# Kernel tuning notes

Hardware: AMD Instinct MI355X
Metric: run time of the kernel (lower is better)

## Reference

```python
import jax, jax.numpy as jnp
import numpy as np

N = 8192
IN = 128   # in_channels
CH = 64    # conv_ch


def setup_inputs() -> dict:
    key = jax.random.key(0)
    ks = jax.random.split(key, 8)
    p = lambda k, shape: jax.random.normal(k, shape, jnp.float32) * 0.02
    return {
        "x": jax.random.normal(ks[0], (N, IN), jnp.float32),
        "edge_index": jax.random.randint(ks[1], (N, N), 0, 2, jnp.int32),
        "W1": p(ks[2], (IN, CH)),      "b1": jnp.zeros((CH,), jnp.float32),
        "W2": p(ks[3], (CH, 2 * CH)),  "b2": jnp.zeros((2 * CH,), jnp.float32),
        "We": p(ks[4], (2 * CH, CH)),  "be": jnp.zeros((CH,), jnp.float32),
        "Wd1": p(ks[5], (2 * CH, CH)), "bd1": jnp.zeros((CH,), jnp.float32),
        "Wd2": p(ks[6], (CH, IN)),     "bd2": jnp.zeros((IN,), jnp.float32),
    }


def _norm_adj(edge_index):
    # PyG GCNConv: A_hat = A + I (self loops appended), sym norm D^-1/2 A_hat D^-1/2
    A = (edge_index != 0).astype(jnp.float32)
    A = A + jnp.eye(A.shape[0], dtype=jnp.float32)
    deg = A.sum(axis=1)
    dinv = jnp.where(deg > 0.0, jax.lax.rsqrt(deg), 0.0)
    return dinv[:, None] * A * dinv[None, :]  # [N, N]


def _gcn(nadj, x, W, b):
    return nadj @ (x @ W) + b


def _lrelu(v):
    return jax.nn.leaky_relu(v, 0.01)  # torch default negative_slope


def reference(x, edge_index, W1, b1, W2, b2, We, be, Wd1, bd1, Wd2, bd2):
    nadj = _norm_adj(edge_index)
    h = _lrelu(_gcn(nadj, x, W1, b1))          # [N, CH]
    z = _lrelu(_gcn(nadj, h, W2, b2))          # [N, 2*CH]
    re = _lrelu(_gcn(nadj, z, We, be))         # [N, CH]
    recon_edge = jax.nn.sigmoid(re @ re.T)     # [N, N]
    xd = _lrelu(_gcn(nadj, z, Wd1, bd1))       # [N, CH]
    x_out = _lrelu(_gcn(nadj, xd, Wd2, bd2))   # [N, IN]
    return (recon_edge, x_out, z)
```

## Files before the change

### kernel.cpp

```cpp
#include <hip/hip_runtime.h>
#include <hip/hip_bf16.h>
#include <stdint.h>

typedef unsigned short u16;
typedef unsigned char u8;
typedef unsigned int u32;
typedef __attribute__((ext_vector_type(8))) short frag8;
typedef __attribute__((ext_vector_type(4))) float f4;

#define N8K 8192
#define SK 8
#define NKT 256


__device__ __forceinline__ u16 f2bf(float f) {
  union { float f; unsigned u; } v; v.f = f;
  return (u16)((v.u + 0x7FFFu + ((v.u >> 16) & 1u)) >> 16);
}
__device__ __forceinline__ float lrelu(float v) { return v > 0.f ? v : 0.01f * v; }

__device__ __forceinline__ void expand4(u32 w, u32& o0, u32& o1) {
  u32 hi = __builtin_amdgcn_perm(0u, 0x00403F00u, w);
  u32 lo = __builtin_amdgcn_perm(0u, 0x00008000u, w);
  o0 = __builtin_amdgcn_perm(hi, lo, 0x05010400u);
  o1 = __builtin_amdgcn_perm(hi, lo, 0x07030602u);
}

__global__ __launch_bounds__(256) void k_deg(const int* __restrict__ e,
                                             u8* __restrict__ at,
                                             float* __restrict__ dinv) {
  int Rt = blockIdx.x;
  int t = threadIdx.x;
  int rl = t & 15;
  int row = Rt * 16 + rl;
  int tg = t >> 4;
  int diagT = row >> 5;
  int cnt = 0;
  __shared__ int cs[256];
  for (int p = 0; p < 16; ++p) {
    int T = tg + 16 * p;
    const int4* src = (const int4*)(e + (size_t)row * N8K + T * 32);
    u32 w[8];
#pragma unroll
    for (int q8 = 0; q8 < 8; ++q8) {
      int4 v = src[q8];
      u32 c0 = (v.x != 0), c1 = (v.y != 0), c2 = (v.z != 0), c3 = (v.w != 0);
      cnt += (int)(c0 + c1 + c2 + c3);
      w[q8] = c0 | (c1 << 8) | (c2 << 16) | (c3 << 24);
    }
    if (T == diagT) {
      int d = row & 31;
      w[d >> 2] += 1u << (8 * (d & 3));
      cnt += 1;
    }
    u8* dst = at + ((size_t)(Rt * NKT + T) * 64 + rl) * 8;
#pragma unroll
    for (int q = 0; q < 4; ++q) {
      uint2 u; u.x = w[2 * q]; u.y = w[2 * q + 1];
      *(uint2*)(dst + (size_t)(16 * q) * 8) = u;
    }
  }
  cs[t] = cnt;
  __syncthreads();
  if (t < 16) {
    int s = 0;
#pragma unroll
    for (int g = 0; g < 16; ++g) s += cs[t + 16 * g];
    dinv[Rt * 16 + t] = 1.0f / sqrtf((float)s);
  }
}

__global__ __launch_bounds__(256, 2) void k_sgemm(const u16* __restrict__ Xt,
                                                  const float* __restrict__ Xf,
                                                  int KT,
                                                  const float* __restrict__ Wa, int wacols,
                                                  const float* __restrict__ Wb,
                                                  const float* __restrict__ dinv,
                                                  u16* __restrict__ Pt) {
  __shared__ __attribute__((aligned(16))) u16 Wt[8 * 4 * 64 * 8];
  int t = threadIdx.x, mt = blockIdx.x;
  int lane = t & 63, wave = t >> 6;
  int units = 8 * KT * 64;
  for (int u = t; u < units; u += 256) {
    int l = u & 63, T = (u >> 6) % KT, nt = (u >> 6) / KT;
    int n = nt * 16 + (l & 15);
    int k0 = T * 32 + (l >> 4) * 8;
    u16 tmp[8];
#pragma unroll
    for (int j = 0; j < 8; ++j) {
      int k = k0 + j;
      float v = (n < wacols) ? Wa[k * wacols + n] : (Wb ? Wb[k * 64 + (n - 64)] : 0.f);
      tmp[j] = f2bf(v);
    }
    *(uint4*)&Wt[(size_t)u * 8] = *(const uint4*)tmp;
  }
  __syncthreads();
  int wm = (wave >> 1) * 64, wn = (wave & 1) * 64;
  int fm = lane & 15, q = lane >> 4;
  f4 acc[4][4];
#pragma unroll
  for (int m = 0; m < 4; ++m)
#pragma unroll
    for (int n = 0; n < 4; ++n) acc[m][n] = (f4){0.f, 0.f, 0.f, 0.f};
  for (int T = 0; T < KT; ++T) {
    frag8 a[4], b[4];
#pragma unroll
    for (int m = 0; m < 4; ++m) {
      int Rt = mt * 8 + (wm >> 4) + m;
      if (Xf) {
        const float* px = Xf + (size_t)(Rt * 16 + fm) * (KT * 32) + T * 32 + q * 8;
        float4 v0 = *(const float4*)px, v1 = *(const float4*)(px + 4);
        u16 tmp[8] = {f2bf(v0.x), f2bf(v0.y), f2bf(v0.z), f2bf(v0.w),
                      f2bf(v1.x), f2bf(v1.y), f2bf(v1.z), f2bf(v1.w)};
        a[m] = *(const frag8*)tmp;
      } else {
        a[m] = *(const frag8*)(Xt + ((size_t)(Rt * KT + T) * 64 + lane) * 8);
      }
    }
#pragma unroll
    for (int n = 0; n < 4; ++n)
      b[n] = *(const frag8*)&Wt[((size_t)(((wn >> 4) + n) * KT + T) * 64 + lane) * 8];
#pragma unroll
    for (int m = 0; m < 4; ++m)
#pragma unroll
      for (int n = 0; n < 4; ++n)
        acc[m][n] = __builtin_amdgcn_mfma_f32_16x16x32_bf16(a[m], b[n], acc[m][n], 0, 0, 0);
  }
#pragma unroll
  for (int m = 0; m < 4; ++m) {
    int ibase = mt * 128 + wm + 16 * m + q * 4;
    float d0 = dinv[ibase], d1 = dinv[ibase + 1], d2 = dinv[ibase + 2], d3 = dinv[ibase + 3];
#pragma unroll
    for (int n = 0; n < 4; ++n) {
      u32 lo = (u32)f2bf(d0 * acc[m][n][0]) | ((u32)f2bf(d1 * acc[m][n][1]) << 16);
      u32 hi = (u32)f2bf(d2 * acc[m][n][2]) | ((u32)f2bf(d3 * acc[m][n][3]) << 16);
      u32 plo = __shfl_xor(lo, 16, 64);
      u32 phi = __shfl_xor(hi, 16, 64);
      if ((q & 1) == 0) {
        uint4 u; u.x = lo; u.y = hi; u.z = plo; u.w = phi;
        int gi = mt * 128 + wm + 16 * m + (q >> 1) * 8;
        int T2 = gi >> 5;
        int lB = fm + 16 * ((gi >> 3) & 3);
        int nt = (wn >> 4) + n;
        *(uint4*)(Pt + ((size_t)(nt * NKT + T2) * 64 + lB) * 8) = u;
      }
    }
  }
}

__global__ __launch_bounds__(256, 3) void k_bgemm(const u8* __restrict__ At,
                                                  const u16* __restrict__ Bt,
                                                  float* __restrict__ Ctmp) {
  int t = threadIdx.x;
  int mt = blockIdx.x, ks = blockIdx.y;
  int lane = t & 63, wave = t >> 6;
  int wm = (wave >> 1) * 64, wn = (wave & 1) * 64;
  f4 acc[4][4];
#pragma unroll
  for (int m = 0; m < 4; ++m)
#pragma unroll
    for (int n = 0; n < 4; ++n) acc[m][n] = (f4){0.f, 0.f, 0.f, 0.f};

  const int T0 = ks * 32;
  const u8*  Ab = At + ((size_t)((mt * 8 + (wm >> 4)) * NKT + T0) * 64 + lane) * 8;
  const u16* Bb = Bt + ((size_t)(((wn >> 4)) * NKT + T0) * 64 + lane) * 8;

#pragma unroll 2
  for (int T = 0; T < 32; ++T) {
    frag8 a[4], b[4];
#pragma unroll
    for (int m = 0; m < 4; ++m) {
      uint2 w = *(const uint2*)(Ab + (size_t)m * (NKT * 512) + (size_t)T * 512);
      uint4 r;
      expand4(w.x, r.x, r.y);
      expand4(w.y, r.z, r.w);
      a[m] = *(const frag8*)&r;
    }
#pragma unroll
    for (int n = 0; n < 4; ++n)
      b[n] = *(const frag8*)(Bb + (size_t)n * (NKT * 512) + (size_t)T * 512);
#pragma unroll
    for (int m = 0; m < 4; ++m)
#pragma unroll
      for (int n = 0; n < 4; ++n)
        acc[m][n] = __builtin_amdgcn_mfma_f32_16x16x32_bf16(a[m], b[n], acc[m][n], 0, 0, 0);
  }

  float* Co = Ctmp + (size_t)ks * (N8K * 128);
  int fm = lane & 15, rbase = (lane >> 4) * 4;
#pragma unroll
  for (int m = 0; m < 4; ++m) {
    int i0 = mt * 128 + wm + 16 * m + rbase;
#pragma unroll
    for (int n = 0; n < 4; ++n) {
      int c = wn + 16 * n + fm;
#pragma unroll
      for (int r = 0; r < 4; ++r) Co[(size_t)(i0 + r) * 128 + c] = acc[m][n][r];
    }
  }
}

__global__ __launch_bounds__(256) void k_epi(const float* __restrict__ Ctmp,
                                             const float* __restrict__ dinv,
                                             const float* __restrict__ bA,
                                             const float* __restrict__ bB,
                                             float* __restrict__ outF,
                                             u16* __restrict__ o1,
                                             u16* __restrict__ o2, int mode) {
  int idx = blockIdx.x * 256 + threadIdx.x;
  int i = idx >> 4, c8 = idx & 15;
  if (mode == 1 && c8 >= 8) return;
  int c0 = c8 * 8;
  float v[8];
#pragma unroll
  for (int j = 0; j < 8; ++j) v[j] = 0.f;
#pragma unroll
  for (int k = 0; k < SK; ++k) {
    const float4* p = (const float4*)(Ctmp + (size_t)k * (N8K * 128) + (size_t)i * 128 + c0);
    float4 x0 = p[0], x1 = p[1];
    v[0] += x0.x; v[1] += x0.y; v[2] += x0.z; v[3] += x0.w;
    v[4] += x1.x; v[5] += x1.y; v[6] += x1.z; v[7] += x1.w;
  }
  float di = dinv[i];
  u16 ob[8];
  if (mode == 3 && c8 >= 8) {
    int cl = c0 - 64;
#pragma unroll
    for (int j = 0; j < 8; ++j) ob[j] = f2bf(lrelu(di * v[j] + bB[cl + j]));
    int T = (c8 - 8) >> 2, l = (i & 15) + 16 * ((c8 - 8) & 3);
    *(uint4*)(o2 + ((size_t)((i >> 4) * 2 + T) * 64 + l) * 8) = *(const uint4*)ob;
    return;
  }
#pragma unroll
  for (int j = 0; j < 8; ++j) v[j] = lrelu(di * v[j] + bA[c0 + j]);
  if (mode == 4) {
    float4* po = (float4*)(outF + (size_t)i * 128 + c0);
    po[0] = (float4){v[0], v[1], v[2], v[3]};
    po[1] = (float4){v[4], v[5], v[6], v[7]};
    return;
  }
#pragma unroll
  for (int j = 0; j < 8; ++j) ob[j] = f2bf(v[j]);
  int KTo = (mode == 2) ? 4 : 2;
  int T = c8 >> 2, l = (i & 15) + 16 * (c8 & 3);
  *(uint4*)(o1 + ((size_t)((i >> 4) * KTo + T) * 64 + l) * 8) = *(const uint4*)ob;
  if (mode == 2) {
    float4* po = (float4*)(outF + (size_t)i * 128 + c0);
    po[0] = (float4){v[0], v[1], v[2], v[3]};
    po[1] = (float4){v[4], v[5], v[6], v[7]};
  }
}

__global__ __launch_bounds__(256, 4) void k_recon(const u16* __restrict__ ret,
                                                  float* __restrict__ out) {
  int t = threadIdx.x;
  int bi = blockIdx.x, bj = blockIdx.y;
  int lane = t & 63, wave = t >> 6;
  int wm = (wave >> 1) * 64, wn = (wave & 1) * 64;
  int fm = lane & 15;
  f4 acc[4][4];
#pragma unroll
  for (int m = 0; m < 4; ++m)
#pragma unroll
    for (int n = 0; n < 4; ++n) acc[m][n] = (f4){0.f, 0.f, 0.f, 0.f};
#pragma unroll
  for (int T = 0; T < 2; ++T) {
    frag8 a[4], b[4];
#pragma unroll
    for (int m = 0; m < 4; ++m)
      a[m] = *(const frag8*)(ret + ((size_t)((bi * 8 + (wm >> 4) + m) * 2 + T) * 64 + lane) * 8);
#pragma unroll
    for (int n = 0; n < 4; ++n)
      b[n] = *(const frag8*)(ret + ((size_t)((bj * 8 + (wn >> 4) + n) * 2 + T) * 64 + lane) * 8);
#pragma unroll
    for (int m = 0; m < 4; ++m)
#pragma unroll
      for (int n = 0; n < 4; ++n)
        acc[m][n] = __builtin_amdgcn_mfma_f32_16x16x32_bf16(a[m], b[n], acc[m][n], 0, 0, 0);
  }
  int rbase = (lane >> 4) * 4;
#pragma unroll
  for (int m = 0; m < 4; ++m) {
#pragma unroll
    for (int n = 0; n < 4; ++n) {
      int gj = bj * 128 + wn + 16 * n + fm;
#pragma unroll
      for (int r = 0; r < 4; ++r) {
        int gi = bi * 128 + wm + 16 * m + rbase + r;
        float ex = __builtin_amdgcn_exp2f(acc[m][n][r] * -1.442695041f);
        out[(size_t)gi * N8K + gj] = __builtin_amdgcn_rcpf(1.0f + ex);
      }
    }
  }
}

extern "C" void kernel_launch(void* const* d_in, const int* in_sizes, int n_in,
                              void* d_out, int out_size, void* d_ws, size_t ws_size,
                              hipStream_t stream) {
  const float* x   = (const float*)d_in[0];
  const int*   e   = (const int*)d_in[1];
  const float* W1  = (const float*)d_in[2];
  const float* b1  = (const float*)d_in[3];
  const float* W2  = (const float*)d_in[4];
  const float* b2  = (const float*)d_in[5];
  const float* We  = (const float*)d_in[6];
  const float* be  = (const float*)d_in[7];
  const float* Wd1 = (const float*)d_in[8];
  const float* bd1 = (const float*)d_in[9];
  const float* Wd2 = (const float*)d_in[10];
  const float* bd2 = (const float*)d_in[11];

  float* out       = (float*)d_out;
  float* out_recon = out;
  float* out_x     = out + 67108864;
  float* out_z     = out + 67108864 + 1048576;

  u8*    at   = (u8*)d_out;
  float* Ctmp = out + 16777216;

  char* ws = (char*)d_ws;
  float* dinv = (float*)(ws);
  u16* Pt  = (u16*)(ws + 32768);
  u16* ht  = (u16*)(ws + 32768 + 2097152);
  u16* zt  = (u16*)(ws + 32768 + 3145728);
  u16* ret = (u16*)(ws + 32768 + 5242880);
  u16* xdt = (u16*)(ws + 32768 + 6291456);

  k_deg<<<512, 256, 0, stream>>>(e, at, dinv);

  k_sgemm<<<64, 256, 0, stream>>>(nullptr, x, 4, W1, 64, nullptr, dinv, Pt);
  k_bgemm<<<dim3(64, SK), 256, 0, stream>>>(at, Pt, Ctmp);
  k_epi<<<512, 256, 0, stream>>>(Ctmp, dinv, b1, nullptr, nullptr, ht, nullptr, 1);

  k_sgemm<<<64, 256, 0, stream>>>(ht, nullptr, 2, W2, 128, nullptr, dinv, Pt);
  k_bgemm<<<dim3(64, SK), 256, 0, stream>>>(at, Pt, Ctmp);
  k_epi<<<512, 256, 0, stream>>>(Ctmp, dinv, b2, nullptr, out_z, zt, nullptr, 2);

  k_sgemm<<<64, 256, 0, stream>>>(zt, nullptr, 4, We, 64, Wd1, dinv, Pt);
  k_bgemm<<<dim3(64, SK), 256, 0, stream>>>(at, Pt, Ctmp);
  k_epi<<<512, 256, 0, stream>>>(Ctmp, dinv, be, bd1, nullptr, ret, xdt, 3);

  k_sgemm<<<64, 256, 0, stream>>>(xdt, nullptr, 2, Wd2, 128, nullptr, dinv, Pt);
  k_bgemm<<<dim3(64, SK), 256, 0, stream>>>(at, Pt, Ctmp);
  k_epi<<<512, 256, 0, stream>>>(Ctmp, dinv, bd2, nullptr, out_x, nullptr, nullptr, 4);

  k_recon<<<dim3(64, 64), 256, 0, stream>>>(ret, out_recon);
}
```

Before: 686.1 us.

## Fuse split-K epilogue with next layer's feature-weight GEMM

Replaces the separate epilogue kernels (split-K reduction, bias, leaky ReLU, bf16 pack) and the following small GEMM with one fused kernel. The activated tile is staged in shared memory and fed directly to MFMA, which removes three launches and the global round-trips for the intermediate h, z and xd buffers. In exchange, the reduction now runs on only 64 blocks instead of 512, which may underuse memory bandwidth on a large GPU.

```diff
diff --git a/kernel.cpp b/kernel.cpp
--- a/kernel.cpp
+++ b/kernel.cpp
@@ -70,18 +70,15 @@
   }
 }
 
-__global__ __launch_bounds__(256, 2) void k_sgemm(const u16* __restrict__ Xt,
-                                                  const float* __restrict__ Xf,
-                                                  int KT,
-                                                  const float* __restrict__ Wa, int wacols,
-                                                  const float* __restrict__ Wb,
-                                                  const float* __restrict__ dinv,
-                                                  u16* __restrict__ Pt) {
+__global__ __launch_bounds__(256, 2) void k_sgemm1(const float* __restrict__ Xf,
+                                                   const float* __restrict__ Wa,
+                                                   const float* __restrict__ dinv,
+                                                   u16* __restrict__ Pt) {
+  const int KT = 4;
   __shared__ __attribute__((aligned(16))) u16 Wt[8 * 4 * 64 * 8];
   int t = threadIdx.x, mt = blockIdx.x;
   int lane = t & 63, wave = t >> 6;
-  int units = 8 * KT * 64;
-  for (int u = t; u < units; u += 256) {
+  for (int u = t; u < 8 * KT * 64; u += 256) {
     int l = u & 63, T = (u >> 6) % KT, nt = (u >> 6) / KT;
     int n = nt * 16 + (l & 15);
     int k0 = T * 32 + (l >> 4) * 8;
@@ -89,7 +86,7 @@
 #pragma unroll
     for (int j = 0; j < 8; ++j) {
       int k = k0 + j;
-      float v = (n < wacols) ? Wa[k * wacols + n] : (Wb ? Wb[k * 64 + (n - 64)] : 0.f);
+      float v = (n < 64) ? Wa[k * 64 + n] : 0.f;
       tmp[j] = f2bf(v);
     }
     *(uint4*)&Wt[(size_t)u * 8] = *(const uint4*)tmp;
@@ -107,15 +104,11 @@
 #pragma unroll
     for (int m = 0; m < 4; ++m) {
       int Rt = mt * 8 + (wm >> 4) + m;
-      if (Xf) {
-        const float* px = Xf + (size_t)(Rt * 16 + fm) * (KT * 32) + T * 32 + q * 8;
-        float4 v0 = *(const float4*)px, v1 = *(const float4*)(px + 4);
-        u16 tmp[8] = {f2bf(v0.x), f2bf(v0.y), f2bf(v0.z), f2bf(v0.w),
-                      f2bf(v1.x), f2bf(v1.y), f2bf(v1.z), f2bf(v1.w)};
-        a[m] = *(const frag8*)tmp;
-      } else {
-        a[m] = *(const frag8*)(Xt + ((size_t)(Rt * KT + T) * 64 + lane) * 8);
-      }
+      const float* px = Xf + (size_t)(Rt * 16 + fm) * 128 + T * 32 + q * 8;
+      float4 v0 = *(const float4*)px, v1 = *(const float4*)(px + 4);
+      u16 tmp[8] = {f2bf(v0.x), f2bf(v0.y), f2bf(v0.z), f2bf(v0.w),
+                    f2bf(v1.x), f2bf(v1.y), f2bf(v1.z), f2bf(v1.w)};
+      a[m] = *(const frag8*)tmp;
     }
 #pragma unroll
     for (int n = 0; n < 4; ++n)
@@ -200,16 +193,132 @@
   }
 }
 
-__global__ __launch_bounds__(256) void k_epi(const float* __restrict__ Ctmp,
-                                             const float* __restrict__ dinv,
-                                             const float* __restrict__ bA,
-                                             const float* __restrict__ bB,
-                                             float* __restrict__ outF,
-                                             u16* __restrict__ o1,
-                                             u16* __restrict__ o2, int mode) {
+__global__ __launch_bounds__(256, 2) void k_fuse(const float* __restrict__ Ctmp,
+                                                 const float* __restrict__ dinv,
+                                                 const float* __restrict__ bE,
+                                                 const float* __restrict__ bE2,
+                                                 float* __restrict__ outZ,
+                                                 u16* __restrict__ retG,
+                                                 int mode,
+                                                 const float* __restrict__ Wa, int wacols,
+                                                 const float* __restrict__ Wb,
+                                                 u16* __restrict__ Pt) {
+  __shared__ __attribute__((aligned(16))) u16 Xs[8 * 4 * 64 * 8];
+  __shared__ __attribute__((aligned(16))) u16 Wt[8 * 4 * 64 * 8];
+  int t = threadIdx.x, mt = blockIdx.x;
+  int lane = t & 63, wave = t >> 6;
+  const int KT = (mode == 2) ? 4 : 2;
+
+  int C8 = (mode == 1) ? 8 : 16;
+  int totalU = 128 * C8;
+  for (int u0 = t; u0 < totalU; u0 += 256) {
+    int i = (mode == 1) ? (u0 >> 3) : (u0 >> 4);
+    int c8 = (mode == 1) ? (u0 & 7) : (u0 & 15);
+    int gi = mt * 128 + i;
+    int c0 = c8 * 8;
+    float v[8];
+#pragma unroll
+    for (int j = 0; j < 8; ++j) v[j] = 0.f;
+#pragma unroll
+    for (int k = 0; k < SK; ++k) {
+      const float4* p = (const float4*)(Ctmp + (size_t)k * (N8K * 128) + (size_t)gi * 128 + c0);
+      float4 x0 = p[0], x1 = p[1];
+      v[0] += x0.x; v[1] += x0.y; v[2] += x0.z; v[3] += x0.w;
+      v[4] += x1.x; v[5] += x1.y; v[6] += x1.z; v[7] += x1.w;
+    }
+    float di = dinv[gi];
+    u16 ob[8];
+    if (mode == 3 && c8 < 8) {
+#pragma unroll
+      for (int j = 0; j < 8; ++j) ob[j] = f2bf(lrelu(di * v[j] + bE[c0 + j]));
+      int T = c8 >> 2, l = (i & 15) + 16 * (c8 & 3);
+      *(uint4*)(retG + ((size_t)((gi >> 4) * 2 + T) * 64 + l) * 8) = *(const uint4*)ob;
+    } else if (mode == 3) {
+      int cl = c0 - 64;
+#pragma unroll
+      for (int j = 0; j < 8; ++j) ob[j] = f2bf(lrelu(di * v[j] + bE2[cl + j]));
+      int cp = c8 - 8;
+      int T = cp >> 2, l = (i & 15) + 16 * (cp & 3);
+      *(uint4*)&Xs[(((i >> 4) * 2 + T) * 64 + l) * 8] = *(const uint4*)ob;
+    } else {
+#pragma unroll
+      for (int j = 0; j < 8; ++j) v[j] = lrelu(di * v[j] + bE[c0 + j]);
+#pragma unroll
+      for (int j = 0; j < 8; ++j) ob[j] = f2bf(v[j]);
+      int T = c8 >> 2, l = (i & 15) + 16 * (c8 & 3);
+      *(uint4*)&Xs[(((i >> 4) * KT + T) * 64 + l) * 8] = *(const uint4*)ob;
+      if (mode == 2) {
+        float4* po = (float4*)(outZ + (size_t)gi * 128 + c0);
+        po[0] = (float4){v[0], v[1], v[2], v[3]};
+        po[1] = (float4){v[4], v[5], v[6], v[7]};
+      }
+    }
+  }
+
+  for (int u = t; u < 8 * KT * 64; u += 256) {
+    int l = u & 63, T = (u >> 6) % KT, nt = (u >> 6) / KT;
+    int n = nt * 16 + (l & 15);
+    int k0 = T * 32 + (l >> 4) * 8;
+    u16 tmp[8];
+#pragma unroll
+    for (int j = 0; j < 8; ++j) {
+      int k = k0 + j;
+      float v = (n < wacols) ? Wa[k * wacols + n] : (Wb ? Wb[k * 64 + (n - 64)] : 0.f);
+      tmp[j] = f2bf(v);
+    }
+    *(uint4*)&Wt[(size_t)u * 8] = *(const uint4*)tmp;
+  }
+  __syncthreads();
+
+  int wm = (wave >> 1) * 64, wn = (wave & 1) * 64;
+  int fm = lane & 15, q = lane >> 4;
+  f4 acc[4][4];
+#pragma unroll
+  for (int m = 0; m < 4; ++m)
+#pragma unroll
+    for (int n = 0; n < 4; ++n) acc[m][n] = (f4){0.f, 0.f, 0.f, 0.f};
+  for (int T = 0; T < KT; ++T) {
+    frag8 a[4], b[4];
+#pragma unroll
+    for (int m = 0; m < 4; ++m)
+      a[m] = *(const frag8*)&Xs[((size_t)(((wm >> 4) + m) * KT + T) * 64 + lane) * 8];
+#pragma unroll
+    for (int n = 0; n < 4; ++n)
+      b[n] = *(const frag8*)&Wt[((size_t)(((wn >> 4) + n) * KT + T) * 64 + lane) * 8];
+#pragma unroll
+    for (int m = 0; m < 4; ++m)
+#pragma unroll
+      for (int n = 0; n < 4; ++n)
+        acc[m][n] = __builtin_amdgcn_mfma_f32_16x16x32_bf16(a[m], b[n], acc[m][n], 0, 0, 0);
+  }
+#pragma unroll
+  for (int m = 0; m < 4; ++m) {
+    int ibase = mt * 128 + wm + 16 * m + q * 4;
+    float d0 = dinv[ibase], d1 = dinv[ibase + 1], d2 = dinv[ibase + 2], d3 = dinv[ibase + 3];
+#pragma unroll
+    for (int n = 0; n < 4; ++n) {
+      u32 lo = (u32)f2bf(d0 * acc[m][n][0]) | ((u32)f2bf(d1 * acc[m][n][1]) << 16);
+      u32 hi = (u32)f2bf(d2 * acc[m][n][2]) | ((u32)f2bf(d3 * acc[m][n][3]) << 16);
+      u32 plo = __shfl_xor(lo, 16, 64);
+      u32 phi = __shfl_xor(hi, 16, 64);
+      if ((q & 1) == 0) {
+        uint4 u; u.x = lo; u.y = hi; u.z = plo; u.w = phi;
+        int gi = mt * 128 + wm + 16 * m + (q >> 1) * 8;
+        int T2 = gi >> 5;
+        int lB = fm + 16 * ((gi >> 3) & 3);
+        int nt = (wn >> 4) + n;
+        *(uint4*)(Pt + ((size_t)(nt * NKT + T2) * 64 + lB) * 8) = u;
+      }
+    }
+  }
+}
+
+__global__ __launch_bounds__(256) void k_epi4(const float* __restrict__ Ctmp,
+                                              const float* __restrict__ dinv,
+                                              const float* __restrict__ bA,
+                                              float* __restrict__ outF) {
   int idx = blockIdx.x * 256 + threadIdx.x;
   int i = idx >> 4, c8 = idx & 15;
-  if (mode == 1 && c8 >= 8) return;
   int c0 = c8 * 8;
   float v[8];
 #pragma unroll
@@ -222,33 +331,11 @@
     v[4] += x1.x; v[5] += x1.y; v[6] += x1.z; v[7] += x1.w;
   }
   float di = dinv[i];
-  u16 ob[8];
-  if (mode == 3 && c8 >= 8) {
-    int cl = c0 - 64;
-#pragma unroll
-    for (int j = 0; j < 8; ++j) ob[j] = f2bf(lrelu(di * v[j] + bB[cl + j]));
-    int T = (c8 - 8) >> 2, l = (i & 15) + 16 * ((c8 - 8) & 3);
-    *(uint4*)(o2 + ((size_t)((i >> 4) * 2 + T) * 64 + l) * 8) = *(const uint4*)ob;
-    return;
-  }
 #pragma unroll
   for (int j = 0; j < 8; ++j) v[j] = lrelu(di * v[j] + bA[c0 + j]);
-  if (mode == 4) {
-    float4* po = (float4*)(outF + (size_t)i * 128 + c0);
-    po[0] = (float4){v[0], v[1], v[2], v[3]};
-    po[1] = (float4){v[4], v[5], v[6], v[7]};
-    return;
-  }
-#pragma unroll
-  for (int j = 0; j < 8; ++j) ob[j] = f2bf(v[j]);
-  int KTo = (mode == 2) ? 4 : 2;
-  int T = c8 >> 2, l = (i & 15) + 16 * (c8 & 3);
-  *(uint4*)(o1 + ((size_t)((i >> 4) * KTo + T) * 64 + l) * 8) = *(const uint4*)ob;
-  if (mode == 2) {
-    float4* po = (float4*)(outF + (size_t)i * 128 + c0);
-    po[0] = (float4){v[0], v[1], v[2], v[3]};
-    po[1] = (float4){v[4], v[5], v[6], v[7]};
-  }
+  float4* po = (float4*)(outF + (size_t)i * 128 + c0);
+  po[0] = (float4){v[0], v[1], v[2], v[3]};
+  po[1] = (float4){v[4], v[5], v[6], v[7]};
 }
 
 __global__ __launch_bounds__(256, 4) void k_recon(const u16* __restrict__ ret,
@@ -321,28 +408,26 @@
   char* ws = (char*)d_ws;
   float* dinv = (float*)(ws);
   u16* Pt  = (u16*)(ws + 32768);
-  u16* ht  = (u16*)(ws + 32768 + 2097152);
-  u16* zt  = (u16*)(ws + 32768 + 3145728);
-  u16* ret = (u16*)(ws + 32768 + 5242880);
-  u16* xdt = (u16*)(ws + 32768 + 6291456);
+  u16* ret = (u16*)(ws + 32768 + 2097152);
 
   k_deg<<<512, 256, 0, stream>>>(e, at, dinv);
 
-  k_sgemm<<<64, 256, 0, stream>>>(nullptr, x, 4, W1, 64, nullptr, dinv, Pt);
+  k_sgemm1<<<64, 256, 0, stream>>>(x, W1, dinv, Pt);
   k_bgemm<<<dim3(64, SK), 256, 0, stream>>>(at, Pt, Ctmp);
-  k_epi<<<512, 256, 0, stream>>>(Ctmp, dinv, b1, nullptr, nullptr, ht, nullptr, 1);
-
-  k_sgemm<<<64, 256, 0, stream>>>(ht, nullptr, 2, W2, 128, nullptr, dinv, Pt);
+
+  k_fuse<<<64, 256, 0, stream>>>(Ctmp, dinv, b1, nullptr, nullptr, nullptr, 1,
+                                 W2, 128, nullptr, Pt);
   k_bgemm<<<dim3(64, SK), 256, 0, stream>>>(at, Pt, Ctmp);
-  k_epi<<<512, 256, 0, stream>>>(Ctmp, dinv, b2, nullptr, out_z, zt, nullptr, 2);
-
-  k_sgemm<<<64, 256, 0, stream>>>(zt, nullptr, 4, We, 64, Wd1, dinv, Pt);
+
+  k_fuse<<<64, 256, 0, stream>>>(Ctmp, dinv, b2, nullptr, out_z, nullptr, 2,
+                                 We, 64, Wd1, Pt);
   k_bgemm<<<dim3(64, SK), 256, 0, stream>>>(at, Pt, Ctmp);
-  k_epi<<<512, 256, 0, stream>>>(Ctmp, dinv, be, bd1, nullptr, ret, xdt, 3);
-
-  k_sgemm<<<64, 256, 0, stream>>>(xdt, nullptr, 2, Wd2, 128, nullptr, dinv, Pt);
+
+  k_fuse<<<64, 256, 0, stream>>>(Ctmp, dinv, be, bd1, nullptr, ret, 3,
+                                 Wd2, 128, nullptr, Pt);
   k_bgemm<<<dim3(64, SK), 256, 0, stream>>>(at, Pt, Ctmp);
-  k_epi<<<512, 256, 0, stream>>>(Ctmp, dinv, bd2, nullptr, out_x, nullptr, nullptr, 4);
+
+  k_epi4<<<512, 256, 0, stream>>>(Ctmp, dinv, bd2, out_x);
 
   k_recon<<<dim3(64, 64), 256, 0, stream>>>(ret, out_recon);
 }
```

Result: no change. 683.6 us (-0.4%).
